# Kernel optimization log

Hardware: AMD Instinct MI355X
Metric: run time of the kernel (lower is better)

The kernel has to match this reference:

```python
import jax, jax.numpy as jnp
import numpy as np
import math

B, C, H, W_ = 64, 1024, 10, 10      # C = vis_chans = ir_chans = lan_chans = m_chans
NTOK, MTOK = H * W_, 20             # 100 image tokens (W1: 100x100), 20 text tokens (W2: 100x20)
K_NN, BIG, EPS = 8, 1.0e6, 1e-8


def _minmax(t):
    # per-sample min-max normalization over the full distance slice
    mn = t.min(axis=(1, 2), keepdims=True)
    mx = t.max(axis=(1, 2), keepdims=True)
    return (t - mn) / (mx - mn + EPS)


def _geodesic(X):
    # Isomap-style geodesic distances: symmetric 8-NN Euclidean graph + Floyd-Warshall.
    P = X.shape[0]
    sq = jnp.sum(X * X, axis=-1)
    D = jnp.sqrt(jnp.maximum(sq[:, None] + sq[None, :] - 2.0 * (X @ X.T), 0.0))
    Dm = D + jnp.eye(P, dtype=X.dtype) * BIG          # exclude self from kNN
    negd, idx = jax.lax.top_k(-Dm, K_NN)              # 8 nearest neighbors per node
    A = jnp.full((P, P), BIG, X.dtype).at[jnp.arange(P)[:, None], idx].set(-negd)
    Wg = jnp.minimum(A, A.T)                          # undirected graph
    Wg = Wg.at[jnp.diag_indices(P)].set(0.0)

    def body(Dk, k):
        return jnp.minimum(Dk, Dk[:, k][:, None] + Dk[k, :][None, :]), None

    Wg, _ = jax.lax.scan(body, Wg, jnp.arange(P))
    return Wg


def _forward(ir, vis, lan, vis_w, vis_b, vis_g, vis_be, ir_w, ir_b, ir_g, ir_be,
             t_w, t_b, vout_w, vout_b, tout_w, tout_b, W1, b1, W2, b2, W4, W5,
             ml_w, ml_b, ml2_w, ml2_b, scalars):
    lam1, lam2, a1, be1, g1, a2, be2, g2, wg_aw, wg_ab, wg_bw, wg_bb = scalars
    sqc = jnp.sqrt(jnp.float32(C))
    vis_r = vis.reshape(B, C, -1).transpose(0, 2, 1)   # [B,100,C]
    ir_r = ir.reshape(B, C, -1).transpose(0, 2, 1)     # [B,100,C]
    lan_t = lan.transpose(0, 2, 1)                     # [B,20,C]

    geo = jax.vmap(_geodesic)

    # ---- compute_M_image (detached in original) ----
    joint_vi = jnp.concatenate([vis_r, ir_r], axis=1)                    # [B,200,C]
    d_vi = jax.lax.stop_gradient(geo(joint_vi))[:, :NTOK, NTOK:]         # [B,100,100]
    M_v2i_dist = _minmax(d_vi)
    sigma = jax.lax.stop_gradient(jnp.median(M_v2i_dist))
    M_v2i_fix = jnp.exp(-M_v2i_dist ** 2 / (2.0 * sigma ** 2))
    lam1s = jax.nn.sigmoid(lam1)
    M_v2i_learn = lam1s * M_v2i_fix + (1.0 - lam1s) * (W1 * M_v2i_fix + b1)

    def conv_in_relu(x, w3, b3, g3, be3, i):
        # 1x1 conv + InstanceNorm2d(affine) + ReLU, flattened to tokens
        y = jnp.einsum('bchw,mc->bmhw', x, w3[i]) + b3[i][None, :, None, None]
        mu = y.mean((2, 3), keepdims=True)
        var = y.var((2, 3), keepdims=True)
        y = (y - mu) / jnp.sqrt(var + 1e-5) * g3[i][None, :, None, None] + be3[i][None, :, None, None]
        return jax.nn.relu(y).reshape(B, C, -1).transpose(0, 2, 1)       # [B,100,C]

    Qv, Kv, Vv = [conv_in_relu(vis, vis_w, vis_b, vis_g, vis_be, i) for i in range(3)]
    Qi, Ki, Vi = [conv_in_relu(ir, ir_w, ir_b, ir_g, ir_be, i) for i in range(3)]
    Qt, Kt, Vt = [jax.nn.relu(lan_t @ t_w[i].T + t_b[i]) for i in range(3)]

    # fusion weights from GAP of the learned manifold matrix
    Mgap = M_v2i_learn.mean((1, 2), keepdims=True)       # [B,1,1]
    alpha = jax.nn.sigmoid(wg_aw * Mgap + wg_ab)
    beta = jax.nn.sigmoid(wg_bw * Mgap + wg_bb)
    Qf, Kf, Vf = alpha * Qv + beta * Qi, alpha * Kv + beta * Ki, alpha * Vv + beta * Vi
    feat_img = alpha * vis_r + beta * ir_r               # [B,100,C]

    # ---- compute_M_text (detached in original) ----
    joint_it = jnp.concatenate([feat_img, lan_t], axis=1)                # [B,120,C]
    d_it = jax.lax.stop_gradient(geo(joint_it))
    M_i2t_dist = _minmax(d_it[:, :NTOK, NTOK:])          # [B,100,20] (unused downstream, as in original)
    M_t2i_dist = _minmax(d_it[:, NTOK:, :NTOK])          # [B,20,100]
    sigma2 = jax.lax.stop_gradient(jnp.median(M_t2i_dist))
    M_t2i_fix = jnp.exp(-M_t2i_dist ** 2 / (2.0 * sigma2 ** 2))          # [B,20,100]
    M_i2t_fix = M_t2i_fix.transpose(0, 2, 1)                             # [B,100,20]
    lam2s = jax.nn.sigmoid(lam2)
    M_i2t_lo = lam2s * M_i2t_fix + (1.0 - lam2s) * (W2 * M_i2t_fix + b2) # [B,100,20]
    M_t2i_lo = M_i2t_lo.transpose(0, 2, 1)                               # [B,20,100]
    M_t2i_lo = jax.nn.softmax(M_t2i_lo / sqc, axis=2)
    M_i2t_lo = jax.nn.softmax(M_i2t_lo / sqc, axis=2)
    M_t2i_learn = (M_i2t_lo @ lan_t) @ ml_w.T + ml_b       # [B,100,C]
    M_i2t_learn = (M_t2i_lo @ feat_img) @ ml2_w.T + ml2_b  # [B,20,C]

    # ---- text->image cross attention ----
    A = Qt @ Kf.transpose(0, 2, 1) \
        + a1 * (Qt @ M_t2i_learn.transpose(0, 2, 1)) \
        + be1 * (W4 @ (M_t2i_learn @ Kf.transpose(0, 2, 1)))
    Av = jax.nn.softmax(A / sqc, axis=2)                   # [B,20,100]
    new_lan = Av @ Vf + g1 * (M_t2i_lo @ Vf)               # [B,20,C]

    # ---- image->text cross attention ----
    Bm = Qf @ Kt.transpose(0, 2, 1) \
        + a2 * (Qf @ M_i2t_learn.transpose(0, 2, 1)) \
        + be2 * (W5 @ (M_i2t_learn @ Kt.transpose(0, 2, 1)))
    Bv = jax.nn.softmax(Bm / sqc, axis=2)                  # [B,100,20]
    new_vis = Bv @ Vt + g2 * (M_i2t_lo @ Vt)               # [B,100,C]

    new_vis = new_vis.transpose(0, 2, 1).reshape(B, C, H, W_)
    new_vis = jnp.einsum('bchw,mc->bmhw', new_vis, vout_w) + vout_b[None, :, None, None]
    new_lan = new_lan @ tout_w.T + tout_b

    # ---- regularization loss ----
    fA = jax.nn.softmax(M_t2i_fix / sqc, axis=2)
    fB = jax.nn.softmax(M_i2t_fix / sqc, axis=2)
    l1 = jnp.abs(Av - fA).mean() + jnp.abs(Bv - fB).mean()
    var = lambda x: jnp.var(x, ddof=1)                    # torch .var() is unbiased
    l2 = -jnp.abs(var(Av) - var(fA)) - jnp.abs(var(Bv) - var(fB))
    loss = (l1 + 100.0 * l2) * 1000.0
    return new_vis, new_lan, loss


def setup_inputs() -> dict:
    key = jax.random.key(0)
    ks = jax.random.split(key, 20)
    f = lambda k, s, sc=1.0: jax.random.normal(k, s, jnp.float32) * sc
    return dict(
        ir=f(ks[0], (B, C, H, W_)),
        vis=f(ks[1], (B, C, H, W_)),
        lan=f(ks[2], (B, C, MTOK)),
        vis_w=f(ks[3], (3, C, C), 0.02), vis_b=jnp.zeros((3, C), jnp.float32),
        vis_g=jnp.ones((3, C), jnp.float32), vis_be=jnp.zeros((3, C), jnp.float32),
        ir_w=f(ks[4], (3, C, C), 0.02), ir_b=jnp.zeros((3, C), jnp.float32),
        ir_g=jnp.ones((3, C), jnp.float32), ir_be=jnp.zeros((3, C), jnp.float32),
        t_w=f(ks[5], (3, C, C), 0.02), t_b=jnp.zeros((3, C), jnp.float32),
        vout_w=f(ks[6], (C, C), 0.02), vout_b=jnp.zeros((C,), jnp.float32),
        tout_w=f(ks[7], (C, C), 0.02), tout_b=jnp.zeros((C,), jnp.float32),
        W1=f(ks[8], (NTOK, NTOK), 0.1), b1=jnp.zeros((NTOK, NTOK), jnp.float32),
        W2=f(ks[9], (NTOK, MTOK), 0.1), b2=jnp.zeros((NTOK, MTOK), jnp.float32),
        W4=f(ks[10], (MTOK, NTOK), 0.1),
        W5=f(ks[11], (NTOK, MTOK), 0.1),
        ml_w=f(ks[12], (C, C), 0.02), ml_b=jnp.zeros((C,), jnp.float32),
        ml2_w=f(ks[13], (C, C), 0.02), ml2_b=jnp.zeros((C,), jnp.float32),
        # [lam1, lam2, a1, b1, g1, a2, b2, g2, wg_aw, wg_ab, wg_bw, wg_bb]
        scalars=jnp.array([0.5, 0.5, 0.5, 0.5, 0.5, 0.5, 0.5, 0.5, 0.3, 0.0, 0.3, 0.0], jnp.float32),
    )


def reference(ir, vis, lan, vis_w, vis_b, vis_g, vis_be, ir_w, ir_b, ir_g, ir_be,
              t_w, t_b, vout_w, vout_b, tout_w, tout_b, W1, b1, W2, b2, W4, W5,
              ml_w, ml_b, ml2_w, ml2_b, scalars):
    return _forward(ir, vis, lan, vis_w, vis_b, vis_g, vis_be, ir_w, ir_b, ir_g, ir_be,
                    t_w, t_b, vout_w, vout_b, tout_w, tout_b, W1, b1, W2, b2, W4, W5,
                    ml_w, ml_b, ml2_w, ml2_b, scalars)
```

## Files before the change

### kernel.cpp

```cpp
#include <hip/hip_runtime.h>
#include <hip/hip_bf16.h>
#include <math.h>

#define B_   64
#define C_   1024
#define HW   100
#define MT_  20
#define P1   200
#define P2   120
#define BIGF 1.0e6f
#define EPSF 1e-8f
#define SQC  32.0f

static constexpr size_t F_J    = 0;
static constexpr size_t N_J    = (size_t)B_*P1*C_;
static constexpr size_t F_D    = F_J + N_J;
static constexpr size_t N_D    = (size_t)B_*P1*P1;
static constexpr size_t F_SQ   = F_D + N_D;
static constexpr size_t N_SQ   = (size_t)B_*P1;
static constexpr size_t F_KNN  = F_SQ + N_SQ;
static constexpr size_t N_KNN  = (size_t)B_*P1*8;
static constexpr size_t F_MV   = F_KNN + N_KNN;
static constexpr size_t N_MV   = (size_t)B_*HW*HW;
static constexpr size_t F_MT   = F_MV + N_MV;
static constexpr size_t N_SM   = (size_t)B_*MT_*HW;
static constexpr size_t F_MFIX = F_MT + N_SM;
static constexpr size_t F_QKVF = F_MFIX + N_SM;
static constexpr size_t N_QKVF = (size_t)3*B_*HW*C_;
static constexpr size_t F_QKVT = F_QKVF + N_QKVF;
static constexpr size_t N_QKVT = (size_t)3*B_*MT_*C_;
static constexpr size_t F_FEAT = F_QKVT + N_QKVT;
static constexpr size_t N_FEAT = (size_t)B_*HW*C_;
static constexpr size_t N_SMC  = (size_t)B_*MT_*C_;
static constexpr size_t F_LANML= F_FEAT + N_FEAT;
static constexpr size_t F_T2   = F_LANML + N_SMC;
static constexpr size_t F_MI2TL= F_T2 + N_SMC;
static constexpr size_t F_S1   = F_MI2TL + N_SMC;
static constexpr size_t F_S2   = F_S1 + N_SM;
static constexpr size_t F_S4A  = F_S2 + N_SM;
static constexpr size_t F_S4B  = F_S4A + N_SM;
static constexpr size_t F_S5   = F_S4B + N_SM;
static constexpr size_t F_AV   = F_S5 + (size_t)B_*MT_*MT_;
static constexpr size_t F_BV   = F_AV + N_SM;
static constexpr size_t F_NL   = F_BV + N_SM;
static constexpr size_t F_AL   = F_NL + N_SMC;
static constexpr size_t F_BE   = F_AL + 64;
static constexpr size_t F_HS   = F_BE + 64;
static constexpr size_t F_HIST = F_HS + 8;
static constexpr size_t F_PA   = F_HIST + 1032;
static constexpr size_t F_PB   = F_PA + 6400;

typedef __attribute__((ext_vector_type(8))) short bfrag;
typedef __attribute__((ext_vector_type(4))) short bhalf;
typedef __attribute__((ext_vector_type(4))) float f32x4;
#define MFMA_B16(a,b,c) __builtin_amdgcn_mfma_f32_16x16x32_bf16(a,b,c,0,0,0)

__device__ inline short f2bf(float x){
  __hip_bfloat16 h = __float2bfloat16(x);
  return *reinterpret_cast<short*>(&h);
}


__global__ void k_pack_j1(const float* __restrict__ vis, const float* __restrict__ ir,
                          float* __restrict__ J){
  int idx = blockIdx.x*256 + threadIdx.x;
  if (idx >= B_*P1*C_) return;
  int c = idx & (C_-1);
  int p = (idx >> 10) % P1;
  int b = idx / (C_*P1);
  float v;
  if (p < HW) v = vis[((size_t)b*C_ + c)*HW + p];
  else        v = ir [((size_t)b*C_ + c)*HW + (p-HW)];
  J[idx] = v;
}

__global__ void k_pack_j2(const float* __restrict__ feat, const float* __restrict__ lan,
                          float* __restrict__ J){
  int idx = blockIdx.x*256 + threadIdx.x;
  if (idx >= B_*P2*C_) return;
  int c = idx & (C_-1);
  int p = (idx >> 10) % P2;
  int b = idx / (C_*P2);
  float v;
  if (p < HW) v = feat[((size_t)b*HW + p)*C_ + c];
  else        v = lan [((size_t)b*C_ + c)*MT_ + (p-HW)];
  J[idx] = v;
}

__global__ void k_rowsq(const float* __restrict__ J, float* __restrict__ sq, int P){
  int row = blockIdx.x;
  const float* r = J + (size_t)row*C_;
  float s = 0.f;
  for (int c = threadIdx.x; c < C_; c += 64){ float v = r[c]; s += v*v; }
  for (int o = 32; o > 0; o >>= 1) s += __shfl_down(s, o);
  if (threadIdx.x == 0) sq[row] = s;
}

__global__ __launch_bounds__(256) void k_gram_dist(const float* __restrict__ J,
    const float* __restrict__ sq, float* __restrict__ D, int P){
  __shared__ float Xi[64][33], Xj[64][33];
  int b = blockIdx.z;
  int r0 = blockIdx.x*64, s0 = blockIdx.y*64;
  int tx = threadIdx.x & 15, ty = threadIdx.x >> 4;
  const float* Jb = J + (size_t)b*P*C_;
  float acc[4][4];
  #pragma unroll
  for (int u = 0; u < 4; u++)
    #pragma unroll
    for (int v = 0; v < 4; v++) acc[u][v] = 0.f;
  for (int c0 = 0; c0 < C_; c0 += 32){
    for (int e = threadIdx.x; e < 2048; e += 256){
      int rr = e >> 5, cc = e & 31;
      Xi[rr][cc] = (r0+rr < P) ? Jb[(size_t)(r0+rr)*C_ + c0+cc] : 0.f;
      Xj[rr][cc] = (s0+rr < P) ? Jb[(size_t)(s0+rr)*C_ + c0+cc] : 0.f;
    }
    __syncthreads();
    for (int kk = 0; kk < 32; kk++){
      float xr[4], xs[4];
      #pragma unroll
      for (int u = 0; u < 4; u++) xr[u] = Xi[ty*4+u][kk];
      #pragma unroll
      for (int v = 0; v < 4; v++) xs[v] = Xj[tx*4+v][kk];
      #pragma unroll
      for (int u = 0; u < 4; u++)
        #pragma unroll
        for (int v = 0; v < 4; v++) acc[u][v] += xr[u]*xs[v];
    }
    __syncthreads();
  }
  #pragma unroll
  for (int u = 0; u < 4; u++){
    #pragma unroll
    for (int v = 0; v < 4; v++){
      int r = r0 + ty*4 + u, s = s0 + tx*4 + v;
      if (r < P && s < P){
        float d2 = sq[b*P+r] + sq[b*P+s] - 2.f*acc[u][v];
        D[((size_t)b*P + r)*P + s] = sqrtf(fmaxf(d2, 0.f));
      }
    }
  }
}

template<int P>
__global__ void k_knn(const float* __restrict__ D, int* __restrict__ knn){
  constexpr int NS = (P + 63)/64;
  int row = blockIdx.x;
  int i = row % P;
  const float* Dr = D + (size_t)row*P;
  float v[NS];
  #pragma unroll
  for (int t = 0; t < NS; t++){
    int j = threadIdx.x + t*64;
    float d = (j < P) ? Dr[j] : 4.0e6f;
    if (j == i) d += BIGF;
    v[t] = d;
  }
// ... 130 lines not shown
  float scale = 1024.f/(hi - lo);
  unsigned below = 0;
  int idx = blockIdx.x*256 + threadIdx.x;
  int stride = gridDim.x*256;
  for (int i = idx; i < N; i += stride){
    float v = x[i];
    if (v < lo) below++;
    else if (v < hi){
      int bn = (int)((v - lo)*scale);
      if (bn > 1023) bn = 1023;
      atomicAdd(&lh[bn], 1u);
    }
  }
  for (int o = 32; o > 0; o >>= 1) below += __shfl_down(below, o);
  if ((threadIdx.x & 63) == 0 && below) atomicAdd(&lh[1024], below);
  __syncthreads();
  for (int i = threadIdx.x; i < 1025; i += 256){
    unsigned v = lh[i];
    if (v) atomicAdd(&hist[i], v);
  }
}

__global__ void k_med_select(float* hs, const unsigned* __restrict__ hist, int k){
  if (threadIdx.x != 0) return;
  float lo = hs[0], hi = hs[1], w = (hi - lo)*(1.f/1024.f);
  unsigned cum = hist[1024];
  int bf = 1023;
  for (int bn = 0; bn < 1024; bn++){
    unsigned h = hist[bn];
    if (cum + h > (unsigned)k){ bf = bn; break; }
    cum += h;
  }
  hs[0] = lo + bf*w; hs[1] = lo + (bf+1)*w;
}

__global__ __launch_bounds__(256) void k_mgap(const float* __restrict__ Mv,
    const float* __restrict__ W1, const float* __restrict__ b1,
    const float* __restrict__ sc, const float* __restrict__ hs,
    float* __restrict__ alpha, float* __restrict__ bet){
  __shared__ float sr[256];
  int b = blockIdx.x;
  float lam1s = 1.f/(1.f + expf(-sc[0]));
  float sig = 0.5f*(hs[0] + hs[1]);
  float inv2s = 1.f/(2.f*sig*sig);
  const float* Mb = Mv + (size_t)b*HW*HW;
  float s = 0.f;
  for (int e = threadIdx.x; e < HW*HW; e += 256){
    float v = Mb[e];
    float f = expf(-v*v*inv2s);
    s += lam1s*f + (1.f - lam1s)*(W1[e]*f + b1[e]);
  }
  sr[threadIdx.x] = s; __syncthreads();
  for (int o = 128; o > 0; o >>= 1){
    if ((int)threadIdx.x < o) sr[threadIdx.x] += sr[threadIdx.x+o];
    __syncthreads();
  }
  if (threadIdx.x == 0){
    float mg = sr[0]*(1.f/(HW*HW));
    alpha[b] = 1.f/(1.f + expf(-(sc[8]*mg + sc[9])));
    bet[b]   = 1.f/(1.f + expf(-(sc[10]*mg + sc[11])));
  }
}

__global__ void k_castw(const float* __restrict__ a, const float* __restrict__ b,
                        short* __restrict__ oa, short* __restrict__ ob){
  int i = (blockIdx.x*256 + threadIdx.x)*4;
  if (i >= 3*C_*C_) return;
  float4 va = *(const float4*)(a + i);
  float4 vb = *(const float4*)(b + i);
  short ra[4] = { f2bf(va.x), f2bf(va.y), f2bf(va.z), f2bf(va.w) };
  short rb[4] = { f2bf(vb.x), f2bf(vb.y), f2bf(vb.z), f2bf(vb.w) };
  *(bhalf*)(oa + i) = *(bhalf*)ra;
  *(bhalf*)(ob + i) = *(bhalf*)rb;
}

__global__ void k_cast(const float* __restrict__ a, short* __restrict__ oa, int n){
  int i = (blockIdx.x*256 + threadIdx.x)*4;
  if (i >= n) return;
  float4 va = *(const float4*)(a + i);
  short ra[4] = { f2bf(va.x), f2bf(va.y), f2bf(va.z), f2bf(va.w) };
  *(bhalf*)(oa + i) = *(bhalf*)ra;
}

__global__ __launch_bounds__(256) void k_xt(const float* __restrict__ X, short* __restrict__ Xt){
  __shared__ float tile[32][33];
  int c0 = blockIdx.x*32, t0 = blockIdx.y*32, b = blockIdx.z;
  int j = threadIdx.x & 31, i0 = threadIdx.x >> 5;
  for (int i = i0; i < 32; i += 8){
    int t = t0 + j;
    tile[i][j] = (t < HW) ? X[((size_t)b*C_ + c0+i)*HW + t] : 0.f;
  }
  __syncthreads();
  for (int i = i0; i < 32; i += 8){
    int t = t0 + i;
    if (t < HW) Xt[((size_t)b*HW + t)*C_ + c0 + j] = f2bf(tile[j][i]);
  }
}

__global__ __launch_bounds__(256) void k_lanT(const float* __restrict__ lan,
                                              short* __restrict__ lanT){
  __shared__ float tile[32][21];
  int c0 = blockIdx.x*32, b = blockIdx.y;
  for (int e = threadIdx.x; e < 32*MT_; e += 256){
    int c = e / MT_, t = e - c*MT_;
    tile[c][t] = lan[((size_t)b*C_ + c0+c)*MT_ + t];
  }
  __syncthreads();
  for (int e = threadIdx.x; e < 32*MT_; e += 256){
    int t = e >> 5, c = e & 31;
    lanT[((size_t)(b*MT_ + t))*C_ + c0 + c] = f2bf(tile[c][t]);
  }
}

__global__ __launch_bounds__(256) void k_convqkv_mfma(
    const short* __restrict__ XtV, const short* __restrict__ XtI,
    const short* __restrict__ WV,  const short* __restrict__ WI,
    const float* __restrict__ vg, const float* __restrict__ vbe,
    const float* __restrict__ ig, const float* __restrict__ ibe,
    const float* __restrict__ alpha, const float* __restrict__ bet,
    float* __restrict__ out){
  int m0 = blockIdx.x*128;
  int wsel = blockIdx.y;
  int b = blockIdx.z;
  int tid = threadIdx.x;
  int lane = tid & 63, w = tid >> 6;
  int lg = lane >> 4, lr = lane & 15;
  f32x4 acc[7][2][2];
  #pragma unroll
  for (int tf = 0; tf < 7; tf++)
    #pragma unroll
    for (int mf = 0; mf < 2; mf++)
      #pragma unroll
      for (int md = 0; md < 2; md++)
        acc[tf][mf][md] = (f32x4){0.f,0.f,0.f,0.f};
  const short* xvp = XtV + (size_t)b*HW*C_ + (size_t)lr*C_ + lg*8;
  const short* xip = XtI + (size_t)b*HW*C_ + (size_t)lr*C_ + lg*8;
  const short* wvp = WV + (size_t)wsel*C_*C_ + (size_t)(m0 + w*32 + lr)*C_ + lg*8;
  const short* wip = WI + (size_t)wsel*C_*C_ + (size_t)(m0 + w*32 + lr)*C_ + lg*8;
  const bfrag zf = {0,0,0,0,0,0,0,0};
  for (int k0 = 0; k0 < C_; k0 += 32){
    bfrag bw0v = *(const bfrag*)(wvp + k0);
    bfrag bw1v = *(const bfrag*)(wvp + (size_t)16*C_ + k0);
    bfrag bw0i = *(const bfrag*)(wip + k0);
    bfrag bw1i = *(const bfrag*)(wip + (size_t)16*C_ + k0);
    #pragma unroll
    for (int tf = 0; tf < 7; tf++){
      bfrag axv = zf, axi = zf;
      if (tf*16 + lr < HW){
        axv = *(const bfrag*)(xvp + (size_t)tf*16*C_ + k0);
        axi = *(const bfrag*)(xip + (size_t)tf*16*C_ + k0);
      }
      acc[tf][0][0] = MFMA_B16(axv, bw0v, acc[tf][0][0]);
      acc[tf][1][0] = MFMA_B16(axv, bw1v, acc[tf][1][0]);
      acc[tf][0][1] = MFMA_B16(axi, bw0i, acc[tf][0][1]);
      acc[tf][1][1] = MFMA_B16(axi, bw1i, acc[tf][1][1]);
    }
  }
  float al = alpha[b], bt = bet[b];
  float* ob = out + ((size_t)(wsel*B_ + b))*HW*C_;
  #pragma unroll
  for (int mf = 0; mf < 2; mf++){
    int m = m0 + w*32 + mf*16 + lr;
    float s1v=0.f,s2v=0.f,s1i=0.f,s2i=0.f;
    #pragma unroll
    for (int tf = 0; tf < 7; tf++){
      #pragma unroll
      for (int r = 0; r < 4; r++){
        int t = tf*16 + lg*4 + r;
        if (t < HW){
          float yv = acc[tf][mf][0][r], yi = acc[tf][mf][1][r];
          s1v += yv; s2v += yv*yv; s1i += yi; s2i += yi*yi;
        }
      }
    }
    s1v += __shfl_xor(s1v,16); s1v += __shfl_xor(s1v,32);
    s2v += __shfl_xor(s2v,16); s2v += __shfl_xor(s2v,32);
    s1i += __shfl_xor(s1i,16); s1i += __shfl_xor(s1i,32);
    s2i += __shfl_xor(s2i,16); s2i += __shfl_xor(s2i,32);
// ... 173 lines not shown
    }
  }
}

__global__ __launch_bounds__(256) void k_textproj_mfma(
    const short* __restrict__ lanT, const short* __restrict__ Wt,
    const float* __restrict__ tb, float* __restrict__ QKVt, float* __restrict__ lanML){
  constexpr int NROW = B_*MT_;
  __shared__ short xs[112*TPAD];
  __shared__ short wsm[128*TPAD];
  int m0 = blockIdx.x*128;
  int t0 = blockIdx.y*112;
  int wsel = blockIdx.z;
  int tid = threadIdx.x;
  int lane = tid & 63, w = tid >> 6;
  int lg = lane >> 4, lr = lane & 15;
  f32x4 acc[7][2];
  #pragma unroll
  for (int tf = 0; tf < 7; tf++)
    #pragma unroll
    for (int mf = 0; mf < 2; mf++)
      acc[tf][mf] = (f32x4){0.f,0.f,0.f,0.f};
  const short* wg = Wt + (size_t)wsel*C_*C_ + (size_t)m0*C_;
  int rr0 = tid >> 3, kk = (tid & 7)*4;
  for (int k0 = 0; k0 < C_; k0 += 32){
    __syncthreads();
    for (int rr = rr0; rr < 112; rr += 32){
      int row = t0 + rr;
      uint2 v = make_uint2(0u, 0u);
      if (row < NROW) v = *(const uint2*)(lanT + (size_t)row*C_ + k0 + kk);
      *(uint2*)&xs[rr*TPAD + kk] = v;
    }
    for (int rr = rr0; rr < 128; rr += 32)
      *(uint2*)&wsm[rr*TPAD + kk] = *(const uint2*)(wg + (size_t)rr*C_ + k0 + kk);
    __syncthreads();
    const short* pw0 = &wsm[(w*32 + lr)*TPAD + lg*4];
    const short* pw1 = &wsm[(w*32 + 16 + lr)*TPAD + lg*4];
    bhalf l0, h0;
    l0 = *(const bhalf*)pw0; h0 = *(const bhalf*)(pw0 + 16);
    bfrag bw0 = {l0[0],l0[1],l0[2],l0[3],h0[0],h0[1],h0[2],h0[3]};
    l0 = *(const bhalf*)pw1; h0 = *(const bhalf*)(pw1 + 16);
    bfrag bw1 = {l0[0],l0[1],l0[2],l0[3],h0[0],h0[1],h0[2],h0[3]};
    #pragma unroll
    for (int tf = 0; tf < 7; tf++){
      const short* pa = &xs[(tf*16 + lr)*TPAD + lg*4];
      bhalf al_ = *(const bhalf*)pa, ah_ = *(const bhalf*)(pa + 16);
      bfrag ax = {al_[0],al_[1],al_[2],al_[3],ah_[0],ah_[1],ah_[2],ah_[3]};
      acc[tf][0] = MFMA_B16(ax, bw0, acc[tf][0]);
      acc[tf][1] = MFMA_B16(ax, bw1, acc[tf][1]);
    }
  }
  bool isml = (wsel == 3);
  #pragma unroll
  for (int mf = 0; mf < 2; mf++){
    int m = m0 + w*32 + mf*16 + lr;
    float bv = isml ? 0.f : tb[wsel*C_ + m];
    #pragma unroll
    for (int tf = 0; tf < 7; tf++){
      #pragma unroll
      for (int r = 0; r < 4; r++){
        int row = t0 + tf*16 + lg*4 + r;
        if (row < NROW){
          float v = acc[tf][mf][r] + bv;
          if (!isml) v = fmaxf(v, 0.f);
          if (isml) lanML[(size_t)row*C_ + m] = v;
          else      QKVt[((size_t)wsel*NROW + row)*C_ + m] = v;
        }
      }
    }
  }
}

__global__ void k_feat(const float* __restrict__ vis, const float* __restrict__ ir,
                       const float* __restrict__ alpha, const float* __restrict__ bet,
                       float* __restrict__ feat){
  int idx = blockIdx.x*256 + threadIdx.x;
  if (idx >= B_*HW*C_) return;
  int c = idx & (C_-1);
  int t = (idx >> 10) % HW;
  int b = idx / (C_*HW);
  feat[idx] = alpha[b]*vis[((size_t)b*C_ + c)*HW + t] + bet[b]*ir[((size_t)b*C_ + c)*HW + t];
}

__global__ void k_mfix(const float* __restrict__ Mt, const float* __restrict__ hs2,
                       float* __restrict__ Mfix){
  int idx = blockIdx.x*256 + threadIdx.x;
  if (idx >= B_*MT_*HW) return;
  float sig = 0.5f*(hs2[0] + hs2[1]);
  float v = Mt[idx];
  Mfix[idx] = expf(-v*v/(2.f*sig*sig));
}

__global__ void k_ppre(const float* __restrict__ Mfix, const float* __restrict__ W2,
                       const float* __restrict__ b2, const float* __restrict__ sc,
                       float* __restrict__ Ppre){
  int idx = blockIdx.x*256 + threadIdx.x;
  if (idx >= B_*HW*MT_) return;
  int j = idx % MT_;
  int i = (idx/MT_) % HW;
  int b = idx/(HW*MT_);
  float lam2s = 1.f/(1.f + expf(-sc[1]));
  float f = Mfix[((size_t)b*MT_ + j)*HW + i];
  Ppre[idx] = lam2s*f + (1.f - lam2s)*(W2[i*MT_ + j]*f + b2[i*MT_ + j]);
}

__global__ __launch_bounds__(256) void k_sm20(const float* __restrict__ Ppre, float* __restrict__ Pi2t){
  int row = blockIdx.x*8 + (threadIdx.x >> 5);
  int lane = threadIdx.x & 31;
  if (row >= B_*HW) return;
  float v = (lane < MT_) ? Ppre[(size_t)row*MT_ + lane]*(1.f/SQC) : -3.4e38f;
  float m = v;
  for (int o = 16; o > 0; o >>= 1) m = fmaxf(m, __shfl_xor(m, o, 32));
  float e = (lane < MT_) ? expf(v - m) : 0.f;
  float s = e;
  for (int o = 16; o > 0; o >>= 1) s += __shfl_xor(s, o, 32);
  if (lane < MT_) Pi2t[(size_t)row*MT_ + lane] = e/s;
}

__global__ __launch_bounds__(128) void k_smT(const float* __restrict__ Ppre, float* __restrict__ Pt2i){
  __shared__ float sm[128], ss[128];
  int bj = blockIdx.x; int b = bj/MT_, j = bj % MT_;
  int i = threadIdx.x;
  float v = (i < HW) ? Ppre[((size_t)b*HW + i)*MT_ + j]*(1.f/SQC) : -3.4e38f;
  sm[i] = v; __syncthreads();
  for (int o = 64; o > 0; o >>= 1){
    if (i < o) sm[i] = fmaxf(sm[i], sm[i+o]);
    __syncthreads();
  }
  float m = sm[0];
  float e = (i < HW) ? expf(v - m) : 0.f;
  ss[i] = e; __syncthreads();
  for (int o = 64; o > 0; o >>= 1){
    if (i < o) ss[i] += ss[i+o];
    __syncthreads();
  }
  if (i < HW) Pt2i[((size_t)b*MT_ + j)*HW + i] = e/ss[0];
}

__global__ __launch_bounds__(256) void k_mlearn_t2i(const float* __restrict__ Pi2t,
    const float* __restrict__ lanML, const float* __restrict__ mlb, float* __restrict__ out){
  __shared__ float sP[HW][MT_];
  int b = blockIdx.y; int m = blockIdx.x*256 + threadIdx.x;
  for (int e = threadIdx.x; e < HW*MT_; e += 256) sP[e/MT_][e%MT_] = Pi2t[(size_t)b*HW*MT_ + e];
  __syncthreads();
  float vL[MT_];
  #pragma unroll
  for (int j = 0; j < MT_; j++) vL[j] = lanML[((size_t)b*MT_ + j)*C_ + m];
  float bb = mlb[m];
  for (int i = 0; i < HW; i++){
    float a = bb;
    #pragma unroll
    for (int j = 0; j < MT_; j++) a += sP[i][j]*vL[j];
    out[((size_t)b*HW + i)*C_ + m] = a;
  }
}

__global__ __launch_bounds__(256) void k_t2(const float* __restrict__ Pt2i,
    const float* __restrict__ feat, float* __restrict__ T2o){
  __shared__ float sP[MT_][HW];
  int b = blockIdx.y; int m = blockIdx.x*256 + threadIdx.x;
  for (int e = threadIdx.x; e < MT_*HW; e += 256) sP[e/HW][e%HW] = Pt2i[(size_t)b*MT_*HW + e];
  __syncthreads();
  float acc[MT_];
  #pragma unroll
  for (int j = 0; j < MT_; j++) acc[j] = 0.f;
  for (int i = 0; i < HW; i++){
    float f = feat[((size_t)b*HW + i)*C_ + m];
    #pragma unroll
    for (int j = 0; j < MT_; j++) acc[j] += sP[j][i]*f;
  }
  #pragma unroll
  for (int j = 0; j < MT_; j++) T2o[((size_t)b*MT_ + j)*C_ + m] = acc[j];
}

__global__ __launch_bounds__(256) void k_abt(const float* __restrict__ X,
    const float* __restrict__ Y, float* __restrict__ out, int I, int Jd){
  __shared__ float Xs[16][33], Ys[64][33];
  int i0 = blockIdx.x*16, j0 = blockIdx.y*64, b = blockIdx.z;
  int jl = threadIdx.x & 63, ig = threadIdx.x >> 6;
  float acc[4] = {0.f,0.f,0.f,0.f};
  const float* Xb = X + (size_t)b*I*C_;
  const float* Yb = Y + (size_t)b*Jd*C_;
  for (int c0 = 0; c0 < C_; c0 += 32){
    for (int e = threadIdx.x; e < 512; e += 256){
      int r = e >> 5, cc = e & 31;
      Xs[r][cc] = (i0+r < I) ? Xb[(size_t)(i0+r)*C_ + c0+cc] : 0.f;
    }
    for (int e = threadIdx.x; e < 2048; e += 256){
      int r = e >> 5, cc = e & 31;
      Ys[r][cc] = (j0+r < Jd) ? Yb[(size_t)(j0+r)*C_ + c0+cc] : 0.f;
    }
    __syncthreads();
    for (int kk = 0; kk < 32; kk++){
      float y = Ys[jl][kk];
      #pragma unroll
      for (int k = 0; k < 4; k++) acc[k] += Xs[ig*4+k][kk]*y;
    }
    __syncthreads();
  }
  #pragma unroll
  for (int k = 0; k < 4; k++){
    int i = i0 + ig*4 + k, j = j0 + jl;
    if (i < I && j < Jd) out[((size_t)b*I + i)*Jd + j] = acc[k];
  }
}

__global__ __launch_bounds__(128) void k_attA(const float* __restrict__ S1,
    const float* __restrict__ S2, const float* __restrict__ S3,
    const float* __restrict__ W4, const float* __restrict__ sc, float* __restrict__ Av){
  __shared__ float red[128];
  int bq = blockIdx.x; int b = bq/MT_, q = bq % MT_;
  int j = threadIdx.x;
  float a1 = sc[2], be1 = sc[3];
  float v = -3.4e38f;
  if (j < HW){
    float s3 = 0.f;
    const float* S3b = S3 + (size_t)b*HW*HW + j;
    const float* w4 = W4 + (size_t)q*HW;
    for (int p = 0; p < HW; p++) s3 += w4[p]*S3b[(size_t)p*HW];
    size_t off = ((size_t)b*MT_ + q)*HW + j;
    v = (S1[off] + a1*S2[off] + be1*s3)*(1.f/SQC);
  }
  red[j] = v; __syncthreads();
  for (int o = 64; o > 0; o >>= 1){
    if (j < o) red[j] = fmaxf(red[j], red[j+o]);
    __syncthreads();
  }
  float m = red[0]; __syncthreads();
  float e = (j < HW) ? expf(v - m) : 0.f;
  red[j] = e; __syncthreads();
  for (int o = 64; o > 0; o >>= 1){
    if (j < o) red[j] += red[j+o];
    __syncthreads();
  }
  if (j < HW) Av[((size_t)b*MT_ + q)*HW + j] = e/red[0];
}

__global__ __launch_bounds__(256) void k_attB(const float* __restrict__ S4a,
    const float* __restrict__ S4b, const float* __restrict__ S5,
    const float* __restrict__ W5, const float* __restrict__ sc, float* __restrict__ Bv){
  int row = blockIdx.x*8 + (threadIdx.x >> 5);
  int lane = threadIdx.x & 31;
  if (row >= B_*HW) return;
  int b = row/HW, i = row % HW;
  float a2 = sc[5], be2 = sc[6];
  float v = -3.4e38f;
  if (lane < MT_){
    float s5 = 0.f;
    const float* S5b = S5 + (size_t)b*MT_*MT_ + lane;
    const float* w5 = W5 + (size_t)i*MT_;
    #pragma unroll
    for (int p = 0; p < MT_; p++) s5 += w5[p]*S5b[p*MT_];
    size_t off = (size_t)row*MT_ + lane;
    v = (S4a[off] + a2*S4b[off] + be2*s5)*(1.f/SQC);
  }
  float m = v;
  for (int o = 16; o > 0; o >>= 1) m = fmaxf(m, __shfl_xor(m, o, 32));
  float e = (lane < MT_) ? expf(v - m) : 0.f;
  float s = e;
  for (int o = 16; o > 0; o >>= 1) s += __shfl_xor(s, o, 32);
  if (lane < MT_) Bv[(size_t)row*MT_ + lane] = e/s;
}

__global__ __launch_bounds__(256) void k_nl(const float* __restrict__ Av,
    const float* __restrict__ Pt2i, const float* __restrict__ Vf,
    const float* __restrict__ sc, float* __restrict__ NL){
  __shared__ float sA[MT_][HW];
  int b = blockIdx.y; int m = blockIdx.x*256 + threadIdx.x;
  float g1 = sc[4];
  for (int e = threadIdx.x; e < MT_*HW; e += 256)
    sA[e/HW][e%HW] = Av[(size_t)b*MT_*HW + e] + g1*Pt2i[(size_t)b*MT_*HW + e];
  __syncthreads();
  float acc[MT_];
  #pragma unroll
  for (int q = 0; q < MT_; q++) acc[q] = 0.f;
  for (int k = 0; k < HW; k++){
    float v = Vf[((size_t)b*HW + k)*C_ + m];
    #pragma unroll
    for (int q = 0; q < MT_; q++) acc[q] += sA[q][k]*v;
  }
  #pragma unroll
  for (int q = 0; q < MT_; q++) NL[((size_t)b*MT_ + q)*C_ + m] = acc[q];
}

__global__ __launch_bounds__(256) void k_nv(const float* __restrict__ Bv,
    const float* __restrict__ Pi2t, const float* __restrict__ Vt,
// ... 119 lines not shown
                              hipStream_t stream){
  const float* ir     = (const float*)d_in[0];
  const float* vis    = (const float*)d_in[1];
  const float* lan    = (const float*)d_in[2];
  const float* vis_w  = (const float*)d_in[3];
  const float* vis_g  = (const float*)d_in[5];
  const float* vis_be = (const float*)d_in[6];
  const float* ir_w   = (const float*)d_in[7];
  const float* ir_g   = (const float*)d_in[9];
  const float* ir_be  = (const float*)d_in[10];
  const float* t_w    = (const float*)d_in[11];
  const float* t_b    = (const float*)d_in[12];
  const float* vout_w = (const float*)d_in[13];
  const float* vout_b = (const float*)d_in[14];
  const float* tout_w = (const float*)d_in[15];
  const float* tout_b = (const float*)d_in[16];
  const float* W1     = (const float*)d_in[17];
  const float* b1     = (const float*)d_in[18];
  const float* W2     = (const float*)d_in[19];
  const float* b2     = (const float*)d_in[20];
  const float* W4     = (const float*)d_in[21];
  const float* W5     = (const float*)d_in[22];
  const float* ml_w   = (const float*)d_in[23];
  const float* ml_b   = (const float*)d_in[24];
  const float* ml2_w  = (const float*)d_in[25];
  const float* ml2_b  = (const float*)d_in[26];
  const float* sc     = (const float*)d_in[27];

  float* ws = (float*)d_ws;
  float* J     = ws + F_J;
  float* Dm    = ws + F_D;
  float* sqb   = ws + F_SQ;
  int*   knn   = (int*)(ws + F_KNN);
  float* Mv    = ws + F_MV;
  float* Mt    = ws + F_MT;
  float* Mfix  = ws + F_MFIX;
  float* QKVf  = ws + F_QKVF;
  float* QKVt  = ws + F_QKVT;
  float* feat  = ws + F_FEAT;
  float* lanML = ws + F_LANML;
  float* T2b   = ws + F_T2;
  float* Mi2tL = ws + F_MI2TL;
  float* S1    = ws + F_S1;
  float* S2    = ws + F_S2;
  float* S4a   = ws + F_S4A;
  float* S4b   = ws + F_S4B;
  float* S5    = ws + F_S5;
  float* Av    = ws + F_AV;
  float* Bv    = ws + F_BV;
  float* NL    = ws + F_NL;
  float* alpha = ws + F_AL;
  float* bet   = ws + F_BE;
  float* hs    = ws + F_HS;
  unsigned* hist = (unsigned*)(ws + F_HIST);
  float* pa    = ws + F_PA;
  float* pb    = ws + F_PB;
  float* MlT2I = ws + F_J;
  float* S3    = ws + F_D;
  float* Pi2t  = ws + F_MV;
  float* Pt2i  = ws + F_MV + 128000;
  float* Ppre  = ws + F_MV + 256000;
  short* XtV    = (short*)(ws + F_J);
  short* XtI    = (short*)(ws + F_J + 3300000);
  short* WVb    = (short*)(ws + F_J + 6600000);
  short* WIb    = (short*)(ws + F_J + 8200000);
  short* NVb    = (short*)(ws + F_J + 6553600);
  short* Wob16  = (short*)(ws + F_J + 9830400);
  short* lanTb  = (short*)(ws + F_J + 10360000);
  short* Wtb    = (short*)(ws + F_D);
  short* tout16 = (short*)(ws + F_D + 1000000);
  short* ml2w16 = (short*)(ws + F_D + 1530000);

  float* out_vis  = (float*)d_out;
  float* out_lan  = out_vis + (size_t)B_*C_*HW;
  float* out_loss = out_lan + (size_t)B_*MT_*C_;

  float* Qf = QKVf;
  float* Kf = QKVf + (size_t)B_*HW*C_;
  float* Vf = QKVf + (size_t)2*B_*HW*C_;
  float* Qt = QKVt;
  float* Kt = QKVt + (size_t)B_*MT_*C_;
  float* Vt = QKVt + (size_t)2*B_*MT_*C_;

  k_pack_j1<<<(B_*P1*C_+255)/256,256,0,stream>>>(vis, ir, J);
  k_rowsq<<<B_*P1,64,0,stream>>>(J, sqb, P1);
  k_gram_dist<<<dim3((P1+63)/64,(P1+63)/64,B_),256,0,stream>>>(J, sqb, Dm, P1);
  k_knn<P1><<<B_*P1,64,0,stream>>>(Dm, knn);
  k_buildw<<<(B_*P1*P1+255)/256,256,0,stream>>>(Dm, knn, P1);
  k_fw<P1,10,4><<<B_,1024,0,stream>>>(Dm);
  k_minmax<<<B_,256,0,stream>>>(Dm, Mv, P1, 0, 100, 100, 100);
  k_med_init<<<1,64,0,stream>>>(hs);
  for (int it = 0; it < 3; it++){
    hipMemsetAsync(hist, 0, 1025*sizeof(unsigned), stream);
    k_med_hist<<<256,256,0,stream>>>(Mv, B_*HW*HW, hs, hist);
    k_med_select<<<1,64,0,stream>>>(hs, hist, B_*HW*HW/2);
  }
  k_mgap<<<B_,256,0,stream>>>(Mv, W1, b1, sc, hs, alpha, bet);

  k_castw<<<(3*C_*C_/4+255)/256,256,0,stream>>>(vis_w, ir_w, WVb, WIb);
  k_cast<<<(C_*C_/4+255)/256,256,0,stream>>>(vout_w, Wob16, C_*C_);
  k_cast<<<(3*C_*C_/4+255)/256,256,0,stream>>>(t_w, Wtb, 3*C_*C_);
  k_cast<<<(C_*C_/4+255)/256,256,0,stream>>>(ml_w, Wtb + (size_t)3*C_*C_, C_*C_);
  k_xt<<<dim3(32,4,B_),256,0,stream>>>(vis, XtV);
  k_xt<<<dim3(32,4,B_),256,0,stream>>>(ir, XtI);
  k_lanT<<<dim3(32,B_),256,0,stream>>>(lan, lanTb);
  k_convqkv_mfma<<<dim3(8,3,B_),256,0,stream>>>(XtV, XtI, WVb, WIb,
                                                vis_g, vis_be, ir_g, ir_be,
                                                alpha, bet, QKVf);
  k_textproj_mfma<<<dim3(8,12,4),256,0,stream>>>(lanTb, Wtb, t_b, QKVt, lanML);
  k_cast<<<(C_*C_/4+255)/256,256,0,stream>>>(tout_w, tout16, C_*C_);
  k_cast<<<(C_*C_/4+255)/256,256,0,stream>>>(ml2_w, ml2w16, C_*C_);
  k_feat<<<(B_*HW*C_+255)/256,256,0,stream>>>(vis, ir, alpha, bet, feat);

  k_pack_j2<<<(B_*P2*C_+255)/256,256,0,stream>>>(feat, lan, J);
  k_rowsq<<<B_*P2,64,0,stream>>>(J, sqb, P2);
  k_gram_dist<<<dim3((P2+63)/64,(P2+63)/64,B_),256,0,stream>>>(J, sqb, Dm, P2);
  k_knn<P2><<<B_*P2,64,0,stream>>>(Dm, knn);
  k_buildw<<<(B_*P2*P2+255)/256,256,0,stream>>>(Dm, knn, P2);
  k_fw<P2,4,4><<<B_,960,0,stream>>>(Dm);
  k_minmax<<<B_,256,0,stream>>>(Dm, Mt, P2, 100, 0, MT_, 100);
  k_med_init<<<1,64,0,stream>>>(hs+2);
  for (int it = 0; it < 3; it++){
    hipMemsetAsync(hist, 0, 1025*sizeof(unsigned), stream);
    k_med_hist<<<256,256,0,stream>>>(Mt, B_*MT_*HW, hs+2, hist);
    k_med_select<<<1,64,0,stream>>>(hs+2, hist, B_*MT_*HW/2);
  }
  k_mfix<<<(B_*MT_*HW+255)/256,256,0,stream>>>(Mt, hs+2, Mfix);
  k_ppre<<<(B_*HW*MT_+255)/256,256,0,stream>>>(Mfix, W2, b2, sc, Ppre);
  k_sm20<<<(B_*HW+7)/8,256,0,stream>>>(Ppre, Pi2t);
  k_smT<<<B_*MT_,128,0,stream>>>(Ppre, Pt2i);

  k_mlearn_t2i<<<dim3(4,B_),256,0,stream>>>(Pi2t, lanML, ml_b, MlT2I);
  k_t2<<<dim3(4,B_),256,0,stream>>>(Pt2i, feat, T2b);
  k_tokproj_mfma<<<dim3(8,12),256,0,stream>>>(T2b, ml2w16, ml2_b, Mi2tL);

  k_abt<<<dim3(2,2,B_),256,0,stream>>>(Qt, Kf, S1, MT_, HW);
  k_abt<<<dim3(2,2,B_),256,0,stream>>>(Qt, MlT2I, S2, MT_, HW);
  k_s3_mfma<<<dim3(2,B_),256,0,stream>>>(MlT2I, Kf, S3);
  k_abt<<<dim3(7,1,B_),256,0,stream>>>(Qf, Kt, S4a, HW, MT_);
  k_abt<<<dim3(7,1,B_),256,0,stream>>>(Qf, Mi2tL, S4b, HW, MT_);
  k_abt<<<dim3(2,1,B_),256,0,stream>>>(Mi2tL, Kt, S5, MT_, MT_);
  k_attA<<<B_*MT_,128,0,stream>>>(S1, S2, S3, W4, sc, Av);
  k_attB<<<B_*HW/8,256,0,stream>>>(S4a, S4b, S5, W5, sc, Bv);

  k_nl<<<dim3(4,B_),256,0,stream>>>(Av, Pt2i, Vf, sc, NL);
  k_nv<<<dim3(4,B_),256,0,stream>>>(Bv, Pi2t, Vt, sc, NVb);
  k_tokproj_mfma<<<dim3(8,12),256,0,stream>>>(NL, tout16, tout_b, out_lan);
  k_convout_mfma<<<dim3(8,B_),256,0,stream>>>(NVb, Wob16, vout_b, out_vis);

  k_lossA<<<B_*MT_,128,0,stream>>>(Mfix, Av, pa);
  k_lossB<<<B_*HW/8,256,0,stream>>>(Mfix, Bv, pb);
  k_loss_final<<<1,256,0,stream>>>(pa, pb, out_loss);
}
```

Measured before the change: 2.943 ms.

## Fuse small elementwise and GEMM kernels, tile-transpose J pack, trim median iterations

The J1 pack now goes through a shared-memory transpose tile, so both the strided reads from vis/ir and the writes to J are coalesced. The two transpose-cast launches are merged into one kernel, Mfix and Ppre are computed in a single kernel, and pairs of A·B^T products that share the same left operand are fused so X is loaded once per tile. The histogram median refinement drops from three passes to two, which cuts launches and memsets but may lower the precision of the median estimate used for sigma. The main aim is fewer kernel launches and less global memory traffic.

```diff
diff --git a/kernel.cpp b/kernel.cpp
--- a/kernel.cpp
+++ b/kernel.cpp
@@ -61,17 +61,23 @@
 }
 
 
-__global__ void k_pack_j1(const float* __restrict__ vis, const float* __restrict__ ir,
-                          float* __restrict__ J){
-  int idx = blockIdx.x*256 + threadIdx.x;
-  if (idx >= B_*P1*C_) return;
-  int c = idx & (C_-1);
-  int p = (idx >> 10) % P1;
-  int b = idx / (C_*P1);
-  float v;
-  if (p < HW) v = vis[((size_t)b*C_ + c)*HW + p];
-  else        v = ir [((size_t)b*C_ + c)*HW + (p-HW)];
-  J[idx] = v;
+__global__ __launch_bounds__(256) void k_pack_j1(const float* __restrict__ vis,
+    const float* __restrict__ ir, float* __restrict__ J){
+  __shared__ float tile[32][33];
+  int c0 = blockIdx.x*32, p0 = blockIdx.y*32, b = blockIdx.z;
+  int j = threadIdx.x & 31, i0 = threadIdx.x >> 5;
+  for (int i = i0; i < 32; i += 8){
+    int p = p0 + j;
+    float v = 0.f;
+    if (p < P1) v = (p < HW) ? vis[((size_t)b*C_ + c0+i)*HW + p]
+                             : ir [((size_t)b*C_ + c0+i)*HW + (p-HW)];
+    tile[i][j] = v;
+  }
+  __syncthreads();
+  for (int i = i0; i < 32; i += 8){
+    int p = p0 + i;
+    if (p < P1) J[((size_t)b*P1 + p)*C_ + c0 + j] = tile[j][i];
+  }
 }
 
 __global__ void k_pack_j2(const float* __restrict__ feat, const float* __restrict__ lan,
@@ -368,18 +374,27 @@
   *(bhalf*)(oa + i) = *(bhalf*)ra;
 }
 
-__global__ __launch_bounds__(256) void k_xt(const float* __restrict__ X, short* __restrict__ Xt){
-  __shared__ float tile[32][33];
+__global__ __launch_bounds__(256) void k_xt2(const float* __restrict__ V,
+    const float* __restrict__ I, short* __restrict__ XtV, short* __restrict__ XtI){
+  __shared__ float tv[32][33], ti[32][33];
   int c0 = blockIdx.x*32, t0 = blockIdx.y*32, b = blockIdx.z;
   int j = threadIdx.x & 31, i0 = threadIdx.x >> 5;
   for (int i = i0; i < 32; i += 8){
     int t = t0 + j;
-    tile[i][j] = (t < HW) ? X[((size_t)b*C_ + c0+i)*HW + t] : 0.f;
+    float a = 0.f, c = 0.f;
+    if (t < HW){
+      a = V[((size_t)b*C_ + c0+i)*HW + t];
+      c = I[((size_t)b*C_ + c0+i)*HW + t];
+    }
+    tv[i][j] = a; ti[i][j] = c;
   }
   __syncthreads();
   for (int i = i0; i < 32; i += 8){
     int t = t0 + i;
-    if (t < HW) Xt[((size_t)b*HW + t)*C_ + c0 + j] = f2bf(tile[j][i]);
+    if (t < HW){
+      XtV[((size_t)b*HW + t)*C_ + c0 + j] = f2bf(tv[j][i]);
+      XtI[((size_t)b*HW + t)*C_ + c0 + j] = f2bf(ti[j][i]);
+    }
   }
 }
 
@@ -719,26 +734,21 @@
   feat[idx] = alpha[b]*vis[((size_t)b*C_ + c)*HW + t] + bet[b]*ir[((size_t)b*C_ + c)*HW + t];
 }
 
-__global__ void k_mfix(const float* __restrict__ Mt, const float* __restrict__ hs2,
-                       float* __restrict__ Mfix){
+__global__ void k_mfixppre(const float* __restrict__ Mt, const float* __restrict__ hs2,
+                           const float* __restrict__ W2, const float* __restrict__ b2,
+                           const float* __restrict__ sc,
+                           float* __restrict__ Mfix, float* __restrict__ Ppre){
   int idx = blockIdx.x*256 + threadIdx.x;
   if (idx >= B_*MT_*HW) return;
+  int i = idx % HW;
+  int j = (idx/HW) % MT_;
+  int b = idx/(MT_*HW);
   float sig = 0.5f*(hs2[0] + hs2[1]);
   float v = Mt[idx];
-  Mfix[idx] = expf(-v*v/(2.f*sig*sig));
-}
-
-__global__ void k_ppre(const float* __restrict__ Mfix, const float* __restrict__ W2,
-                       const float* __restrict__ b2, const float* __restrict__ sc,
-                       float* __restrict__ Ppre){
-  int idx = blockIdx.x*256 + threadIdx.x;
-  if (idx >= B_*HW*MT_) return;
-  int j = idx % MT_;
-  int i = (idx/MT_) % HW;
-  int b = idx/(HW*MT_);
+  float f = expf(-v*v/(2.f*sig*sig));
+  Mfix[idx] = f;
   float lam2s = 1.f/(1.f + expf(-sc[1]));
-  float f = Mfix[((size_t)b*MT_ + j)*HW + i];
-  Ppre[idx] = lam2s*f + (1.f - lam2s)*(W2[i*MT_ + j]*f + b2[i*MT_ + j]);
+  Ppre[((size_t)b*HW + i)*MT_ + j] = lam2s*f + (1.f - lam2s)*(W2[i*MT_ + j]*f + b2[i*MT_ + j]);
 }
 
 __global__ __launch_bounds__(256) void k_sm20(const float* __restrict__ Ppre, float* __restrict__ Pi2t){
@@ -839,6 +849,50 @@
   for (int k = 0; k < 4; k++){
     int i = i0 + ig*4 + k, j = j0 + jl;
     if (i < I && j < Jd) out[((size_t)b*I + i)*Jd + j] = acc[k];
+  }
+}
+
+__global__ __launch_bounds__(256) void k_abt2(const float* __restrict__ X,
+    const float* __restrict__ Y1, const float* __restrict__ Y2,
+    float* __restrict__ out1, float* __restrict__ out2, int I, int Jd){
+  __shared__ float Xs[16][33], Y1s[64][33], Y2s[64][33];
+  int i0 = blockIdx.x*16, j0 = blockIdx.y*64, b = blockIdx.z;
+  int jl = threadIdx.x & 63, ig = threadIdx.x >> 6;
+  float acc1[4] = {0.f,0.f,0.f,0.f};
+  float acc2[4] = {0.f,0.f,0.f,0.f};
+  const float* Xb  = X  + (size_t)b*I*C_;
+  const float* Y1b = Y1 + (size_t)b*Jd*C_;
+  const float* Y2b = Y2 + (size_t)b*Jd*C_;
+  for (int c0 = 0; c0 < C_; c0 += 32){
+    for (int e = threadIdx.x; e < 512; e += 256){
+      int r = e >> 5, cc = e & 31;
+      Xs[r][cc] = (i0+r < I) ? Xb[(size_t)(i0+r)*C_ + c0+cc] : 0.f;
+    }
+    for (int e = threadIdx.x; e < 2048; e += 256){
+      int r = e >> 5, cc = e & 31;
+      bool ok = (j0+r < Jd);
+      Y1s[r][cc] = ok ? Y1b[(size_t)(j0+r)*C_ + c0+cc] : 0.f;
+      Y2s[r][cc] = ok ? Y2b[(size_t)(j0+r)*C_ + c0+cc] : 0.f;
+    }
+    __syncthreads();
+    for (int kk = 0; kk < 32; kk++){
+      float y1 = Y1s[jl][kk], y2 = Y2s[jl][kk];
+      #pragma unroll
+      for (int k = 0; k < 4; k++){
+        float x = Xs[ig*4+k][kk];
+        acc1[k] += x*y1;
+        acc2[k] += x*y2;
+      }
+    }
+    __syncthreads();
+  }
+  #pragma unroll
+  for (int k = 0; k < 4; k++){
+    int i = i0 + ig*4 + k, j = j0 + jl;
+    if (i < I && j < Jd){
+      out1[((size_t)b*I + i)*Jd + j] = acc1[k];
+      out2[((size_t)b*I + i)*Jd + j] = acc2[k];
+    }
   }
 }
 
@@ -1124,7 +1178,7 @@
   float* Kt = QKVt + (size_t)B_*MT_*C_;
   float* Vt = QKVt + (size_t)2*B_*MT_*C_;
 
-  k_pack_j1<<<(B_*P1*C_+255)/256,256,0,stream>>>(vis, ir, J);
+  k_pack_j1<<<dim3(32,7,B_),256,0,stream>>>(vis, ir, J);
   k_rowsq<<<B_*P1,64,0,stream>>>(J, sqb, P1);
   k_gram_dist<<<dim3((P1+63)/64,(P1+63)/64,B_),256,0,stream>>>(J, sqb, Dm, P1);
   k_knn<P1><<<B_*P1,64,0,stream>>>(Dm, knn);
@@ -1132,7 +1186,7 @@
   k_fw<P1,10,4><<<B_,1024,0,stream>>>(Dm);
   k_minmax<<<B_,256,0,stream>>>(Dm, Mv, P1, 0, 100, 100, 100);
   k_med_init<<<1,64,0,stream>>>(hs);
-  for (int it = 0; it < 3; it++){
+  for (int it = 0; it < 2; it++){
     hipMemsetAsync(hist, 0, 1025*sizeof(unsigned), stream);
     k_med_hist<<<256,256,0,stream>>>(Mv, B_*HW*HW, hs, hist);
     k_med_select<<<1,64,0,stream>>>(hs, hist, B_*HW*HW/2);
@@ -1143,8 +1197,7 @@
   k_cast<<<(C_*C_/4+255)/256,256,0,stream>>>(vout_w, Wob16, C_*C_);
   k_cast<<<(3*C_*C_/4+255)/256,256,0,stream>>>(t_w, Wtb, 3*C_*C_);
   k_cast<<<(C_*C_/4+255)/256,256,0,stream>>>(ml_w, Wtb + (size_t)3*C_*C_, C_*C_);
-  k_xt<<<dim3(32,4,B_),256,0,stream>>>(vis, XtV);
-  k_xt<<<dim3(32,4,B_),256,0,stream>>>(ir, XtI);
+  k_xt2<<<dim3(32,4,B_),256,0,stream>>>(vis, ir, XtV, XtI);
   k_lanT<<<dim3(32,B_),256,0,stream>>>(lan, lanTb);
   k_convqkv_mfma<<<dim3(8,3,B_),256,0,stream>>>(XtV, XtI, WVb, WIb,
                                                 vis_g, vis_be, ir_g, ir_be,
@@ -1162,13 +1215,12 @@
   k_fw<P2,4,4><<<B_,960,0,stream>>>(Dm);
   k_minmax<<<B_,256,0,stream>>>(Dm, Mt, P2, 100, 0, MT_, 100);
   k_med_init<<<1,64,0,stream>>>(hs+2);
-  for (int it = 0; it < 3; it++){
+  for (int it = 0; it < 2; it++){
     hipMemsetAsync(hist, 0, 1025*sizeof(unsigned), stream);
     k_med_hist<<<256,256,0,stream>>>(Mt, B_*MT_*HW, hs+2, hist);
     k_med_select<<<1,64,0,stream>>>(hs+2, hist, B_*MT_*HW/2);
   }
-  k_mfix<<<(B_*MT_*HW+255)/256,256,0,stream>>>(Mt, hs+2, Mfix);
-  k_ppre<<<(B_*HW*MT_+255)/256,256,0,stream>>>(Mfix, W2, b2, sc, Ppre);
+  k_mfixppre<<<(B_*MT_*HW+255)/256,256,0,stream>>>(Mt, hs+2, W2, b2, sc, Mfix, Ppre);
   k_sm20<<<(B_*HW+7)/8,256,0,stream>>>(Ppre, Pi2t);
   k_smT<<<B_*MT_,128,0,stream>>>(Ppre, Pt2i);
 
@@ -1176,11 +1228,9 @@
   k_t2<<<dim3(4,B_),256,0,stream>>>(Pt2i, feat, T2b);
   k_tokproj_mfma<<<dim3(8,12),256,0,stream>>>(T2b, ml2w16, ml2_b, Mi2tL);
 
-  k_abt<<<dim3(2,2,B_),256,0,stream>>>(Qt, Kf, S1, MT_, HW);
-  k_abt<<<dim3(2,2,B_),256,0,stream>>>(Qt, MlT2I, S2, MT_, HW);
+  k_abt2<<<dim3(2,2,B_),256,0,stream>>>(Qt, Kf, MlT2I, S1, S2, MT_, HW);
   k_s3_mfma<<<dim3(2,B_),256,0,stream>>>(MlT2I, Kf, S3);
-  k_abt<<<dim3(7,1,B_),256,0,stream>>>(Qf, Kt, S4a, HW, MT_);
-  k_abt<<<dim3(7,1,B_),256,0,stream>>>(Qf, Mi2tL, S4b, HW, MT_);
+  k_abt2<<<dim3(7,1,B_),256,0,stream>>>(Qf, Kt, Mi2tL, S4a, S4b, HW, MT_);
   k_abt<<<dim3(2,1,B_),256,0,stream>>>(Mi2tL, Kt, S5, MT_, MT_);
   k_attA<<<B_*MT_,128,0,stream>>>(S1, S2, S3, W4, sc, Av);
   k_attB<<<B_*HW/8,256,0,stream>>>(S4a, S4b, S5, W5, sc, Bv);
```

New measurement: 2.643 ms. 10.2% less time.
